# Performance work log

Measured on AMD Instinct MI355X. Metric: run time of the kernel, lower is better.

## Reference

```python
import jax, jax.numpy as jnp
import numpy as np

DIM = 192
HEADS = 6
HD = DIM // HEADS
WS = 7
R = 128  # low-rank projected sequence length
N_FULL = 3136  # 56*56
B = 32


def setup_inputs() -> dict:
    key = jax.random.key(0)
    ks = jax.random.split(key, 9)
    s = 0.02
    return {
        "x": jax.random.normal(ks[0], (2048, WS * WS, DIM), dtype=jnp.float32),
        "qkv_w": jax.random.normal(ks[1], (3 * DIM, DIM), dtype=jnp.float32) * s,
        "qkv_b": jax.random.normal(ks[2], (3 * DIM,), dtype=jnp.float32) * s,
        "E_w": jax.random.normal(ks[3], (R, N_FULL), dtype=jnp.float32) * s,
        "E_b": jax.random.normal(ks[4], (R,), dtype=jnp.float32) * s,
        "F_w": jax.random.normal(ks[5], (R, N_FULL), dtype=jnp.float32) * s,
        "F_b": jax.random.normal(ks[6], (R,), dtype=jnp.float32) * s,
        "proj_w": jax.random.normal(ks[7], (DIM, DIM), dtype=jnp.float32) * s,
        "proj_b": jax.random.normal(ks[8], (DIM,), dtype=jnp.float32) * s,
        "h": 56,
        "w": 56,
    }


def reference(x, qkv_w, qkv_b, E_w, E_b, F_w, F_b, proj_w, proj_b, h, w):
    C = x.shape[-1]
    # window_reverse: (nW*B, ws*ws, C) -> (B, H*W, C)
    xw = x.reshape(-1, WS, WS, C)
    b = xw.shape[0] // ((h // WS) * (w // WS))
    xm = xw.reshape(b, h // WS, w // WS, WS, WS, C)
    xm = xm.transpose(0, 1, 3, 2, 4, 5).reshape(b, h * w, C)
    n = h * w
    scale = 1.0 / np.sqrt(HD)

    qkv = (xm @ qkv_w.T + qkv_b).reshape(b, n, 3, HEADS, HD)
    qkv = qkv.transpose(2, 0, 3, 1, 4)  # (3, b, heads, n, hd)
    q, k, v = qkv[0] * scale, qkv[1], qkv[2]

    # Linformer low-rank projection along sequence: (b,h,n,d) -> (b,h,R,d)
    k_low = jnp.einsum('bhnd,kn->bhkd', k, E_w) + E_b[None, None, :, None]
    v_low = jnp.einsum('bhnd,kn->bhkd', v, F_w) + F_b[None, None, :, None]

    attn = jnp.einsum('bhnd,bhkd->bhnk', q, k_low)  # (b, heads, n, R)
    attn = jax.nn.softmax(attn, axis=-1)

    out = jnp.einsum('bhnk,bhkd->bhnd', attn, v_low)
    out = out.transpose(0, 2, 1, 3).reshape(b, n, C)
    out = out @ proj_w.T + proj_b
    return out
```

## Files before the change

kernel.cpp:

```cpp
#include <hip/hip_runtime.h>

typedef __bf16 bf16;
typedef bf16 bf16x8 __attribute__((ext_vector_type(8)));
typedef bf16 bf16x4 __attribute__((ext_vector_type(4)));
typedef float f32x4 __attribute__((ext_vector_type(4)));

#define MFMA16(a,b,c) __builtin_amdgcn_mfma_f32_16x16x32_bf16(a,b,c,0,0,0)

#define NSEQ 3136
#define CDIM 192

__device__ inline bf16x8 cvt8(float4 a, float4 b) {
  bf16x8 r;
  r[0]=(bf16)a.x; r[1]=(bf16)a.y; r[2]=(bf16)a.z; r[3]=(bf16)a.w;
  r[4]=(bf16)b.x; r[5]=(bf16)b.y; r[6]=(bf16)b.z; r[7]=(bf16)b.w;
  return r;
}

__device__ inline bf16x4 cvt4(float4 a) {
  bf16x4 r;
  r[0]=(bf16)a.x; r[1]=(bf16)a.y; r[2]=(bf16)a.z; r[3]=(bf16)a.w;
  return r;
}

__global__ void k_convert(const float* __restrict__ qkv_w, const float* __restrict__ E_w,
                          const float* __restrict__ F_w, const float* __restrict__ proj_w,
                          bf16* __restrict__ qkvw, bf16* __restrict__ EF, bf16* __restrict__ projw) {
  int i4 = blockIdx.x * blockDim.x + threadIdx.x;
  const int tot4 = 950272 / 4;
  for (; i4 < tot4; i4 += gridDim.x * blockDim.x) {
    int i = i4 * 4;
    float4 f;
    bf16* dst;
    if (i < 110592)      { f = *(const float4*)(qkv_w + i);            dst = qkvw + i; }
    else if (i < 512000) { f = *(const float4*)(E_w + (i - 110592));   dst = EF + (i - 110592); }
    else if (i < 913408) { f = *(const float4*)(F_w + (i - 512000));   dst = EF + (i - 110592); }
    else                 { f = *(const float4*)(proj_w + (i - 913408)); dst = projw + (i - 913408); }
    *(bf16x4*)dst = cvt4(f);
  }
}

__global__ void k_rowsum(const float* __restrict__ E_w, const float* __restrict__ F_w,
                         float* __restrict__ rowsums) {
  __shared__ float red[4];
  int row = blockIdx.x;
  const float* src = (row < 128) ? (E_w + (long)row * NSEQ) : (F_w + (long)(row - 128) * NSEQ);
  float s = 0.f;
  for (int i = threadIdx.x; i < 784; i += 256) {
    float4 f = *(const float4*)(src + i * 4);
    s += f.x + f.y + f.z + f.w;
  }
  for (int off = 32; off; off >>= 1) s += __shfl_xor(s, off);
  if ((threadIdx.x & 63) == 0) red[threadIdx.x >> 6] = s;
  __syncthreads();
  if (threadIdx.x == 0) rowsums[row] = red[0] + red[1] + red[2] + red[3];
}

__global__ void k_xT(const float* __restrict__ x, bf16* __restrict__ xmT) {
  __shared__ bf16 tile[64][196];
  int blk = blockIdx.x;
  int b = blk / 49, n0 = (blk % 49) * 64;
  int tid = threadIdx.x;
  for (int e = tid; e < 3072; e += 256) {
    int row = e / 48, c4 = e % 48;
    int n = n0 + row;
    int r = n / 56, cc = n % 56;
    long srcrow = (long)(b * 64 + (r / 7) * 8 + (cc / 7)) * 49 + (r % 7) * 7 + (cc % 7);
    float4 f = *(const float4*)(x + srcrow * 192 + c4 * 4);
    *(bf16x4*)&tile[row][c4 * 4] = cvt4(f);
  }
  __syncthreads();
  for (int e = tid; e < 1536; e += 256) {
    int c = e >> 3, k = e & 7;
    bf16x8 v;
    for (int jj = 0; jj < 8; jj++) v[jj] = tile[k * 8 + jj][c];
    *(bf16x8*)(xmT + ((long)b * 192 + c) * NSEQ + n0 + k * 8) = v;
  }
}

__launch_bounds__(512)
__global__ void k_xlow(const bf16* __restrict__ EF, const bf16* __restrict__ xmT,
                       float* __restrict__ partial) {
  __shared__ bf16 As[256][72];
  __shared__ bf16 Bs[192][72];
  int idx = blockIdx.x;
  int s = idx % 7, b = idx / 7;
  int kbase = s * 448;
  int tid = threadIdx.x;
  int wid = tid >> 6, lane = tid & 63;
  int wm = wid >> 2, wn = wid & 3;
  int lrow = lane & 15, hi = lane >> 4, lk = hi * 8;
  f32x4 zero = {0.f, 0.f, 0.f, 0.f};
  f32x4 acc[8][3];
  for (int i = 0; i < 8; i++) for (int j = 0; j < 3; j++) acc[i][j] = zero;
  for (int k0 = 0; k0 < 448; k0 += 64) {
    for (int i = 0; i < 4; i++) {
      int unit = i * 512 + tid;
      int row = unit >> 3, koff = (unit & 7) * 8;
      *(bf16x8*)&As[row][koff] = *(const bf16x8*)(EF + (long)row * NSEQ + kbase + k0 + koff);
    }
    for (int i = 0; i < 3; i++) {
      int unit = i * 512 + tid;
      int row = unit >> 3, koff = (unit & 7) * 8;
      *(bf16x8*)&Bs[row][koff] = *(const bf16x8*)(xmT + ((long)b * 192 + row) * NSEQ + kbase + k0 + koff);
    }
    __syncthreads();
    for (int ks = 0; ks < 2; ks++) {
      bf16x8 af[8], bfv[3];
      for (int i = 0; i < 8; i++) af[i]  = *(bf16x8*)&As[wm * 128 + 16 * i + lrow][ks * 32 + lk];
      for (int j = 0; j < 3; j++) bfv[j] = *(bf16x8*)&Bs[wn * 48 + 16 * j + lrow][ks * 32 + lk];
      for (int i = 0; i < 8; i++) for (int j = 0; j < 3; j++) acc[i][j] = MFMA16(af[i], bfv[j], acc[i][j]);
    }
    __syncthreads();
  }
  float* P = partial + (long)idx * 49152;
  for (int i = 0; i < 8; i++) for (int j = 0; j < 3; j++) for (int rr = 0; rr < 4; rr++) {
    int rl = wm * 128 + 16 * i + hi * 4 + rr;
    int cl = wn * 48 + 16 * j + lrow;
    P[rl * 192 + cl] = acc[i][j][rr];
  }
}

__global__ void k_reduce(const float* __restrict__ partial, bf16* __restrict__ el_fl) {
  int blk = blockIdx.x;
  int b = blk / 48, ch = blk % 48;
  long e = (long)ch * 1024 + threadIdx.x * 4;
  const float* P = partial + (long)b * 7 * 49152 + e;
  float4 sum = {0.f, 0.f, 0.f, 0.f};
  for (int s = 0; s < 7; s++) {
    float4 f = *(const float4*)(P + (long)s * 49152);
    sum.x += f.x; sum.y += f.y; sum.z += f.z; sum.w += f.w;
  }
  *(bf16x4*)(el_fl + (long)b * 49152 + e) = cvt4(sum);
}

__launch_bounds__(256)
__global__ void k_lowproj(const bf16* __restrict__ el_fl, const bf16* __restrict__ qkvw,
                          const float* __restrict__ qkv_b, const float* __restrict__ E_b,
                          const float* __restrict__ F_b, const float* __restrict__ rowsums,
                          bf16* __restrict__ k_low, bf16* __restrict__ v_lowT) {
  __shared__ bf16 As[64][200];
  __shared__ bf16 Bs[64][200];
  int idx = blockIdx.x;
  int b = idx / 12, rem = idx % 12;
  int type = rem / 6; rem %= 6;
  int bm, bn;
  if (type == 0) { bm = rem / 3; bn = rem % 3; }
  else           { bm = rem / 2; bn = rem % 2; }
  int m0 = bm * 64, n0 = bn * 64;
  int tid = threadIdx.x;
  int wid = tid >> 6, lane = tid & 63;
  int wm = wid >> 1, wn = wid & 1;
  int lrow = lane & 15, lk = (lane >> 4) * 8;
  int srow = tid >> 2, skoff = (tid & 3) * 16;
  const bf16* Ap; const bf16* Bp;
  if (type == 0) {
    Ap = el_fl + ((long)b * 256 + m0 + srow) * 192 + skoff;
    Bp = qkvw + (long)(192 + n0 + srow) * 192 + skoff;
  } else {
    Ap = qkvw + (long)(384 + m0 + srow) * 192 + skoff;
    Bp = el_fl + ((long)b * 256 + 128 + n0 + srow) * 192 + skoff;
  }
  for (int kk = 0; kk < 192; kk += 64) {
    *(bf16x8*)&As[srow][kk + skoff]     = *(const bf16x8*)(Ap + kk);
    *(bf16x8*)&As[srow][kk + skoff + 8] = *(const bf16x8*)(Ap + kk + 8);
    *(bf16x8*)&Bs[srow][kk + skoff]     = *(const bf16x8*)(Bp + kk);
    *(bf16x8*)&Bs[srow][kk + skoff + 8] = *(const bf16x8*)(Bp + kk + 8);
  }
  __syncthreads();
  f32x4 zero = {0.f, 0.f, 0.f, 0.f};
  f32x4 acc[2][2];
  for (int i = 0; i < 2; i++) for (int j = 0; j < 2; j++) acc[i][j] = zero;
  for (int ks = 0; ks < 6; ks++) {
    bf16x8 af[2], bfv[2];
    for (int i = 0; i < 2; i++) af[i]  = *(bf16x8*)&As[wm * 32 + 16 * i + lrow][ks * 32 + lk];
    for (int j = 0; j < 2; j++) bfv[j] = *(bf16x8*)&Bs[wn * 32 + 16 * j + lrow][ks * 32 + lk];
    for (int i = 0; i < 2; i++) for (int j = 0; j < 2; j++) acc[i][j] = MFMA16(af[i], bfv[j], acc[i][j]);
  }
  if (type == 0) {
    for (int i = 0; i < 2; i++) for (int j = 0; j < 2; j++) for (int rr = 0; rr < 4; rr++) {
      int kr = m0 + wm * 32 + 16 * i + (lane >> 4) * 4 + rr;
      int c = n0 + wn * 32 + 16 * j + lrow;
      float v = acc[i][j][rr] + rowsums[kr] * qkv_b[192 + c] + E_b[kr];
      k_low[((long)b * 128 + kr) * 192 + c] = (bf16)v;
    }
  } else {
    for (int i = 0; i < 2; i++) for (int j = 0; j < 2; j++) for (int rr = 0; rr < 4; rr++) {
      int c = m0 + wm * 32 + 16 * i + (lane >> 4) * 4 + rr;
      int kr = n0 + wn * 32 + 16 * j + lrow;
      float v = acc[i][j][rr] + rowsums[128 + kr] * qkv_b[384 + c] + F_b[kr];
      v_lowT[((long)b * 192 + c) * 128 + kr] = (bf16)v;
    }
  }
}

__launch_bounds__(256)
__global__ void k_qgemm2(const float* __restrict__ x, const bf16* __restrict__ qkvw,
                         const float* __restrict__ qkv_b, bf16* __restrict__ q) {
  __shared__ bf16 As[128][104];
  __shared__ bf16 Bs[192][200];
  long g0 = (long)blockIdx.x * 128;
  int tid = threadIdx.x;
  int wid = tid >> 6, lane = tid & 63;
  int lrow = lane & 15, lk = (lane >> 4) * 8;
  {
    int koff = (tid & 3) * 48;
    for (int r0 = 0; r0 < 192; r0 += 64) {
      int row = r0 + (tid >> 2);
      const bf16* Bp = qkvw + (long)row * 192 + koff;
      for (int m = 0; m < 6; m++)
        *(bf16x8*)&Bs[row][koff + 8 * m] = *(const bf16x8*)(Bp + 8 * m);
    }
  }
  int arow = tid >> 1, half = tid & 1;
  long g = g0 + arow;
  int b = (int)(g / NSEQ), n = (int)(g % NSEQ);
  int r = n / 56, cc = n % 56;
  long srcrow = (long)(b * 64 + (r / 7) * 8 + (cc / 7)) * 49 + (r % 7) * 7 + (cc % 7);
  const float* Ap = x + srcrow * 192 + half * 48;
  f32x4 zero = {0.f, 0.f, 0.f, 0.f};
  f32x4 acc[2][12];
  for (int i = 0; i < 2; i++) for (int j = 0; j < 12; j++) acc[i][j] = zero;
  for (int k0 = 0; k0 < 192; k0 += 96) {
    for (int m = 0; m < 3; m++) {
      const float4* xp = (const float4*)(Ap + k0 + 16 * m);
      float4 f0 = xp[0], f1 = xp[1];
      float4 f2 = xp[2], f3 = xp[3];
      *(bf16x8*)&As[arow][half * 48 + 16 * m] = cvt8(f0, f1);
      *(bf16x8*)&As[arow][half * 48 + 16 * m + 8] = cvt8(f2, f3);
    }
    __syncthreads();
    for (int ks = 0; ks < 3; ks++) {
      bf16x8 af[2];
      for (int i = 0; i < 2; i++) af[i] = *(bf16x8*)&As[wid * 32 + 16 * i + lrow][ks * 32 + lk];
      for (int j = 0; j < 12; j++) {
        bf16x8 bv = *(bf16x8*)&Bs[16 * j + lrow][k0 + ks * 32 + lk];
        acc[0][j] = MFMA16(af[0], bv, acc[0][j]);
        acc[1][j] = MFMA16(af[1], bv, acc[1][j]);
      }
    }
    __syncthreads();
  }
  const float scale = 0.17677669529663687f;
  for (int i = 0; i < 2; i++) for (int j = 0; j < 12; j++) for (int rr = 0; rr < 4; rr++) {
    long grow = g0 + wid * 32 + 16 * i + (lane >> 4) * 4 + rr;
    int c = 16 * j + lrow;
    float v = (acc[i][j][rr] + qkv_b[c]) * scale;
    q[grow * 192 + c] = (bf16)v;
  }
}

__launch_bounds__(256)
__global__ void k_attn(const bf16* __restrict__ q, const bf16* __restrict__ k_low,
                       const bf16* __restrict__ v_lowT, bf16* __restrict__ out_att) {
  __shared__ bf16 Ks[128][40];
  __shared__ bf16 Vs[32][136];
  __shared__ bf16 Ps[4][16][136];
  int idx = blockIdx.x;
  int nt = idx % 49, bh = idx / 49;
  int h = bh % 6, b = bh / 6;
  int n0 = nt * 64;
  int tid = threadIdx.x;
  int wid = tid >> 6, lane = tid & 63;
  int lrow = lane & 15, hi = lane >> 4, lk = hi * 8;
  {
    int row = tid >> 1, koff = (tid & 1) * 16;
    const bf16* src = k_low + ((long)b * 128 + row) * 192 + h * 32 + koff;
    *(bf16x8*)&Ks[row][koff] = *(const bf16x8*)src;
    *(bf16x8*)&Ks[row][koff + 8] = *(const bf16x8*)(src + 8);
  }
  {
    int row = tid >> 3, koff = (tid & 7) * 16;
    const bf16* src = v_lowT + ((long)b * 192 + h * 32 + row) * 128 + koff;
    *(bf16x8*)&Vs[row][koff] = *(const bf16x8*)src;
    *(bf16x8*)&Vs[row][koff + 8] = *(const bf16x8*)(src + 8);
  }
  int nrow = n0 + wid * 16 + lrow;
  bf16x8 qf = *(const bf16x8*)(q + ((long)b * NSEQ + nrow) * 192 + h * 32 + lk);
  __syncthreads();
  f32x4 zero = {0.f, 0.f, 0.f, 0.f};
  f32x4 s[8];
  for (int f = 0; f < 8; f++) {
    bf16x8 kf = *(bf16x8*)&Ks[16 * f + lrow][lk];
    s[f] = MFMA16(kf, qf, zero);
  }
  float m = s[0][0];
  for (int f = 0; f < 8; f++) for (int rr = 0; rr < 4; rr++) m = fmaxf(m, s[f][rr]);
  m = fmaxf(m, __shfl_xor(m, 16));
  m = fmaxf(m, __shfl_xor(m, 32));
  float sum = 0.f;
  for (int f = 0; f < 8; f++) for (int rr = 0; rr < 4; rr++) {
    float p = __expf(s[f][rr] - m);
    s[f][rr] = p; sum += p;
  }
  sum += __shfl_xor(sum, 16);
  sum += __shfl_xor(sum, 32);
  float inv = 1.0f / sum;
  for (int f = 0; f < 8; f++) {
    bf16x4 pv;
    for (int rr = 0; rr < 4; rr++) pv[rr] = (bf16)(s[f][rr] * inv);
    *(bf16x4*)&Ps[wid][lrow][16 * f + hi * 4] = pv;
  }
  __syncthreads();
  f32x4 o[2];
  o[0] = zero; o[1] = zero;
  for (int ks = 0; ks < 4; ks++) {
    bf16x8 pf = *(bf16x8*)&Ps[wid][lrow][ks * 32 + lk];
    for (int j = 0; j < 2; j++) {
      bf16x8 vf = *(bf16x8*)&Vs[16 * j + lrow][ks * 32 + lk];
      o[j] = MFMA16(pf, vf, o[j]);
    }
  }
  for (int j = 0; j < 2; j++) for (int rr = 0; rr < 4; rr++) {
    int nn = n0 + wid * 16 + hi * 4 + rr;
    out_att[((long)b * NSEQ + nn) * 192 + h * 32 + 16 * j + lrow] = (bf16)o[j][rr];
  }
}

__launch_bounds__(256)
__global__ void k_proj(const bf16* __restrict__ oa, const bf16* __restrict__ projw,
                       const float* __restrict__ proj_b, float* __restrict__ out) {
  __shared__ bf16 As[128][104];
  __shared__ bf16 Bs[192][200];
  long g0 = (long)blockIdx.x * 128;
  int tid = threadIdx.x;
  int wid = tid >> 6, lane = tid & 63;
  int lrow = lane & 15, lk = (lane >> 4) * 8;
  {
    int koff = (tid & 3) * 48;
    for (int r0 = 0; r0 < 192; r0 += 64) {
      int row = r0 + (tid >> 2);
      const bf16* Bp = projw + (long)row * 192 + koff;
      for (int m = 0; m < 6; m++)
        *(bf16x8*)&Bs[row][koff + 8 * m] = *(const bf16x8*)(Bp + 8 * m);
    }
  }
  int arow = tid >> 1, half = tid & 1;
  const bf16* Ap = oa + (g0 + arow) * 192 + half * 48;
  f32x4 zero = {0.f, 0.f, 0.f, 0.f};
  f32x4 acc[2][12];
  for (int i = 0; i < 2; i++) for (int j = 0; j < 12; j++) acc[i][j] = zero;
  for (int k0 = 0; k0 < 192; k0 += 96) {
    for (int m = 0; m < 6; m++)
      *(bf16x8*)&As[arow][half * 48 + 8 * m] = *(const bf16x8*)(Ap + k0 + 8 * m);
    __syncthreads();
    for (int ks = 0; ks < 3; ks++) {
      bf16x8 af[2];
      for (int i = 0; i < 2; i++) af[i] = *(bf16x8*)&As[wid * 32 + 16 * i + lrow][ks * 32 + lk];
      for (int j = 0; j < 12; j++) {
        bf16x8 bv = *(bf16x8*)&Bs[16 * j + lrow][k0 + ks * 32 + lk];
        acc[0][j] = MFMA16(af[0], bv, acc[0][j]);
        acc[1][j] = MFMA16(af[1], bv, acc[1][j]);
      }
    }
    __syncthreads();
  }
  for (int i = 0; i < 2; i++) for (int j = 0; j < 12; j++) for (int rr = 0; rr < 4; rr++) {
    long grow = g0 + wid * 32 + 16 * i + (lane >> 4) * 4 + rr;
    int c = 16 * j + lrow;
    out[grow * 192 + c] = acc[i][j][rr] + proj_b[c];
  }
}

extern "C" void kernel_launch(void* const* d_in, const int* in_sizes, int n_in,
                              void* d_out, int out_size, void* d_ws, size_t ws_size,
                              hipStream_t stream) {
  const float* x      = (const float*)d_in[0];
  const float* qkv_w  = (const float*)d_in[1];
  const float* qkv_b  = (const float*)d_in[2];
  const float* E_w    = (const float*)d_in[3];
  const float* E_b    = (const float*)d_in[4];
  const float* F_w    = (const float*)d_in[5];
  const float* F_b    = (const float*)d_in[6];
  const float* proj_w = (const float*)d_in[7];
  const float* proj_b = (const float*)d_in[8];
  float* out = (float*)d_out;

  char* ws = (char*)d_ws;
  size_t off = 0;
  auto alloc = [&](size_t bytes) { char* p = ws + off; off += (bytes + 255) & ~(size_t)255; return p; };
  bf16* qkvw     = (bf16*)alloc((size_t)110592 * 2);
  bf16* EF       = (bf16*)alloc((size_t)802816 * 2);
  bf16* projw    = (bf16*)alloc((size_t)36864 * 2);
  float* rowsums = (float*)alloc((size_t)256 * 4);
  bf16* xmT      = (bf16*)alloc((size_t)32 * 192 * NSEQ * 2);
  float* partial = (float*)alloc((size_t)224 * 49152 * 4);
  bf16* q        = (bf16*)partial;
  bf16* el_fl    = (bf16*)alloc((size_t)32 * 256 * 192 * 2);
  bf16* k_low    = (bf16*)alloc((size_t)32 * 128 * 192 * 2);
  bf16* v_lowT   = (bf16*)alloc((size_t)32 * 192 * 128 * 2);
  bf16* out_att  = xmT;

  k_convert<<<dim3(480), dim3(256), 0, stream>>>(qkv_w, E_w, F_w, proj_w, qkvw, EF, projw);
  k_rowsum<<<dim3(256), dim3(256), 0, stream>>>(E_w, F_w, rowsums);
  k_xT<<<dim3(32 * 49), dim3(256), 0, stream>>>(x, xmT);
  k_xlow<<<dim3(224), dim3(512), 0, stream>>>(EF, xmT, partial);
  k_reduce<<<dim3(1536), dim3(256), 0, stream>>>(partial, el_fl);
  k_lowproj<<<dim3(384), dim3(256), 0, stream>>>(el_fl, qkvw, qkv_b, E_b, F_b, rowsums, k_low, v_lowT);
  k_qgemm2<<<dim3(784), dim3(256), 0, stream>>>(x, qkvw, qkv_b, q);
  k_attn<<<dim3(32 * 6 * 49), dim3(256), 0, stream>>>(q, k_low, v_lowT, out_att);
  k_proj<<<dim3(784), dim3(256), 0, stream>>>(out_att, projw, proj_b, out);
}
```

Measured before the change: 300.5 us.

## Fuse Q projection into window-transpose kernel and merge weight prep kernels

Merges the weight conversion and rowsum kernels into one launch, and fuses the Q-projection GEMM into the window-reverse transpose kernel so x is read once from global memory and reused from shared memory. q now gets its own buffer instead of aliasing the partial buffer. k_low is stored head-major so attention loads contiguous per-head rows. This cuts launch count and a second full read of x, but the fused kernel uses more shared memory and a smaller 64-row tile, which may lower occupancy.

```diff
diff --git a/kernel.cpp b/kernel.cpp
--- a/kernel.cpp
+++ b/kernel.cpp
@@ -23,44 +23,51 @@
   return r;
 }
 
-__global__ void k_convert(const float* __restrict__ qkv_w, const float* __restrict__ E_w,
-                          const float* __restrict__ F_w, const float* __restrict__ proj_w,
-                          bf16* __restrict__ qkvw, bf16* __restrict__ EF, bf16* __restrict__ projw) {
-  int i4 = blockIdx.x * blockDim.x + threadIdx.x;
-  const int tot4 = 950272 / 4;
-  for (; i4 < tot4; i4 += gridDim.x * blockDim.x) {
-    int i = i4 * 4;
-    float4 f;
-    bf16* dst;
-    if (i < 110592)      { f = *(const float4*)(qkv_w + i);            dst = qkvw + i; }
-    else if (i < 512000) { f = *(const float4*)(E_w + (i - 110592));   dst = EF + (i - 110592); }
-    else if (i < 913408) { f = *(const float4*)(F_w + (i - 512000));   dst = EF + (i - 110592); }
-    else                 { f = *(const float4*)(proj_w + (i - 913408)); dst = projw + (i - 913408); }
-    *(bf16x4*)dst = cvt4(f);
-  }
-}
-
-__global__ void k_rowsum(const float* __restrict__ E_w, const float* __restrict__ F_w,
-                         float* __restrict__ rowsums) {
-  __shared__ float red[4];
-  int row = blockIdx.x;
-  const float* src = (row < 128) ? (E_w + (long)row * NSEQ) : (F_w + (long)(row - 128) * NSEQ);
-  float s = 0.f;
-  for (int i = threadIdx.x; i < 784; i += 256) {
-    float4 f = *(const float4*)(src + i * 4);
-    s += f.x + f.y + f.z + f.w;
-  }
-  for (int off = 32; off; off >>= 1) s += __shfl_xor(s, off);
-  if ((threadIdx.x & 63) == 0) red[threadIdx.x >> 6] = s;
-  __syncthreads();
-  if (threadIdx.x == 0) rowsums[row] = red[0] + red[1] + red[2] + red[3];
-}
-
-__global__ void k_xT(const float* __restrict__ x, bf16* __restrict__ xmT) {
+__global__ void k_prep(const float* __restrict__ qkv_w, const float* __restrict__ E_w,
+                       const float* __restrict__ F_w, const float* __restrict__ proj_w,
+                       bf16* __restrict__ qkvw, bf16* __restrict__ EF, bf16* __restrict__ projw,
+                       float* __restrict__ rowsums) {
+  if (blockIdx.x < 256) {
+    __shared__ float red[4];
+    int row = blockIdx.x;
+    const float* src = (row < 128) ? (E_w + (long)row * NSEQ) : (F_w + (long)(row - 128) * NSEQ);
+    float s = 0.f;
+    for (int i = threadIdx.x; i < 784; i += 256) {
+      float4 f = *(const float4*)(src + i * 4);
+      s += f.x + f.y + f.z + f.w;
+    }
+    for (int off = 32; off; off >>= 1) s += __shfl_xor(s, off);
+    if ((threadIdx.x & 63) == 0) red[threadIdx.x >> 6] = s;
+    __syncthreads();
+    if (threadIdx.x == 0) rowsums[row] = red[0] + red[1] + red[2] + red[3];
+  } else {
+    int i4 = (blockIdx.x - 256) * blockDim.x + threadIdx.x;
+    const int tot4 = 950272 / 4;
+    const int stride = 480 * 256;
+    for (; i4 < tot4; i4 += stride) {
+      int i = i4 * 4;
+      float4 f;
+      bf16* dst;
+      if (i < 110592)      { f = *(const float4*)(qkv_w + i);            dst = qkvw + i; }
+      else if (i < 512000) { f = *(const float4*)(E_w + (i - 110592));   dst = EF + (i - 110592); }
+      else if (i < 913408) { f = *(const float4*)(F_w + (i - 512000));   dst = EF + (i - 110592); }
+      else                 { f = *(const float4*)(proj_w + (i - 913408)); dst = projw + (i - 913408); }
+      *(bf16x4*)dst = cvt4(f);
+    }
+  }
+}
+
+__launch_bounds__(256)
+__global__ void k_xTq(const float* __restrict__ x, const bf16* __restrict__ qkvw,
+                      const float* __restrict__ qkv_b, bf16* __restrict__ xmT,
+                      bf16* __restrict__ q) {
   __shared__ bf16 tile[64][196];
+  __shared__ bf16 Bs[192][104];
   int blk = blockIdx.x;
   int b = blk / 49, n0 = (blk % 49) * 64;
   int tid = threadIdx.x;
+  int wid = tid >> 6, lane = tid & 63;
+  int lrow = lane & 15, hi = lane >> 4, lk = hi * 8;
   for (int e = tid; e < 3072; e += 256) {
     int row = e / 48, c4 = e % 48;
     int n = n0 + row;
@@ -69,12 +76,46 @@
     float4 f = *(const float4*)(x + srcrow * 192 + c4 * 4);
     *(bf16x4*)&tile[row][c4 * 4] = cvt4(f);
   }
-  __syncthreads();
+  for (int u = tid; u < 2304; u += 256) {
+    int row = u / 12, koff = (u % 12) * 8;
+    *(bf16x8*)&Bs[row][koff] = *(const bf16x8*)(qkvw + (long)row * 192 + koff);
+  }
+  __syncthreads();
+  f32x4 zero = {0.f, 0.f, 0.f, 0.f};
+  f32x4 acc[12];
+  for (int j = 0; j < 12; j++) acc[j] = zero;
+  for (int ks = 0; ks < 3; ks++) {
+    bf16x8 af = *(bf16x8*)&tile[wid * 16 + lrow][ks * 32 + lk];
+    for (int j = 0; j < 12; j++) {
+      bf16x8 bv = *(bf16x8*)&Bs[16 * j + lrow][ks * 32 + lk];
+      acc[j] = MFMA16(af, bv, acc[j]);
+    }
+  }
   for (int e = tid; e < 1536; e += 256) {
     int c = e >> 3, k = e & 7;
     bf16x8 v;
     for (int jj = 0; jj < 8; jj++) v[jj] = tile[k * 8 + jj][c];
     *(bf16x8*)(xmT + ((long)b * 192 + c) * NSEQ + n0 + k * 8) = v;
+  }
+  __syncthreads();
+  for (int u = tid; u < 2304; u += 256) {
+    int row = u / 12, koff = (u % 12) * 8;
+    *(bf16x8*)&Bs[row][koff] = *(const bf16x8*)(qkvw + (long)row * 192 + 96 + koff);
+  }
+  __syncthreads();
+  for (int ks = 0; ks < 3; ks++) {
+    bf16x8 af = *(bf16x8*)&tile[wid * 16 + lrow][96 + ks * 32 + lk];
+    for (int j = 0; j < 12; j++) {
+      bf16x8 bv = *(bf16x8*)&Bs[16 * j + lrow][ks * 32 + lk];
+      acc[j] = MFMA16(af, bv, acc[j]);
+    }
+  }
+  const float scale = 0.17677669529663687f;
+  for (int j = 0; j < 12; j++) for (int rr = 0; rr < 4; rr++) {
+    int rl = wid * 16 + hi * 4 + rr;
+    int c = 16 * j + lrow;
+    float v = (acc[j][rr] + qkv_b[c]) * scale;
+    q[((long)b * NSEQ + n0 + rl) * 192 + c] = (bf16)v;
   }
 }
 
@@ -138,7 +179,7 @@
 __global__ void k_lowproj(const bf16* __restrict__ el_fl, const bf16* __restrict__ qkvw,
                           const float* __restrict__ qkv_b, const float* __restrict__ E_b,
                           const float* __restrict__ F_b, const float* __restrict__ rowsums,
-                          bf16* __restrict__ k_low, bf16* __restrict__ v_lowT) {
+                          bf16* __restrict__ k_lowH, bf16* __restrict__ v_lowT) {
   __shared__ bf16 As[64][200];
   __shared__ bf16 Bs[64][200];
   int idx = blockIdx.x;
@@ -182,7 +223,7 @@
       int kr = m0 + wm * 32 + 16 * i + (lane >> 4) * 4 + rr;
       int c = n0 + wn * 32 + 16 * j + lrow;
       float v = acc[i][j][rr] + rowsums[kr] * qkv_b[192 + c] + E_b[kr];
-      k_low[((long)b * 128 + kr) * 192 + c] = (bf16)v;
+      k_lowH[(((long)b * 6 + (c >> 5)) * 128 + kr) * 32 + (c & 31)] = (bf16)v;
     }
   } else {
     for (int i = 0; i < 2; i++) for (int j = 0; j < 2; j++) for (int rr = 0; rr < 4; rr++) {
@@ -195,63 +236,7 @@
 }
 
 __launch_bounds__(256)
-__global__ void k_qgemm2(const float* __restrict__ x, const bf16* __restrict__ qkvw,
-                         const float* __restrict__ qkv_b, bf16* __restrict__ q) {
-  __shared__ bf16 As[128][104];
-  __shared__ bf16 Bs[192][200];
-  long g0 = (long)blockIdx.x * 128;
-  int tid = threadIdx.x;
-  int wid = tid >> 6, lane = tid & 63;
-  int lrow = lane & 15, lk = (lane >> 4) * 8;
-  {
-    int koff = (tid & 3) * 48;
-    for (int r0 = 0; r0 < 192; r0 += 64) {
-      int row = r0 + (tid >> 2);
-      const bf16* Bp = qkvw + (long)row * 192 + koff;
-      for (int m = 0; m < 6; m++)
-        *(bf16x8*)&Bs[row][koff + 8 * m] = *(const bf16x8*)(Bp + 8 * m);
-    }
-  }
-  int arow = tid >> 1, half = tid & 1;
-  long g = g0 + arow;
-  int b = (int)(g / NSEQ), n = (int)(g % NSEQ);
-  int r = n / 56, cc = n % 56;
-  long srcrow = (long)(b * 64 + (r / 7) * 8 + (cc / 7)) * 49 + (r % 7) * 7 + (cc % 7);
-  const float* Ap = x + srcrow * 192 + half * 48;
-  f32x4 zero = {0.f, 0.f, 0.f, 0.f};
-  f32x4 acc[2][12];
-  for (int i = 0; i < 2; i++) for (int j = 0; j < 12; j++) acc[i][j] = zero;
-  for (int k0 = 0; k0 < 192; k0 += 96) {
-    for (int m = 0; m < 3; m++) {
-      const float4* xp = (const float4*)(Ap + k0 + 16 * m);
-      float4 f0 = xp[0], f1 = xp[1];
-      float4 f2 = xp[2], f3 = xp[3];
-      *(bf16x8*)&As[arow][half * 48 + 16 * m] = cvt8(f0, f1);
-      *(bf16x8*)&As[arow][half * 48 + 16 * m + 8] = cvt8(f2, f3);
-    }
-    __syncthreads();
-    for (int ks = 0; ks < 3; ks++) {
-      bf16x8 af[2];
-      for (int i = 0; i < 2; i++) af[i] = *(bf16x8*)&As[wid * 32 + 16 * i + lrow][ks * 32 + lk];
-      for (int j = 0; j < 12; j++) {
-        bf16x8 bv = *(bf16x8*)&Bs[16 * j + lrow][k0 + ks * 32 + lk];
-        acc[0][j] = MFMA16(af[0], bv, acc[0][j]);
-        acc[1][j] = MFMA16(af[1], bv, acc[1][j]);
-      }
-    }
-    __syncthreads();
-  }
-  const float scale = 0.17677669529663687f;
-  for (int i = 0; i < 2; i++) for (int j = 0; j < 12; j++) for (int rr = 0; rr < 4; rr++) {
-    long grow = g0 + wid * 32 + 16 * i + (lane >> 4) * 4 + rr;
-    int c = 16 * j + lrow;
-    float v = (acc[i][j][rr] + qkv_b[c]) * scale;
-    q[grow * 192 + c] = (bf16)v;
-  }
-}
-
-__launch_bounds__(256)
-__global__ void k_attn(const bf16* __restrict__ q, const bf16* __restrict__ k_low,
+__global__ void k_attn(const bf16* __restrict__ q, const bf16* __restrict__ k_lowH,
                        const bf16* __restrict__ v_lowT, bf16* __restrict__ out_att) {
   __shared__ bf16 Ks[128][40];
   __shared__ bf16 Vs[32][136];
@@ -265,7 +250,7 @@
   int lrow = lane & 15, hi = lane >> 4, lk = hi * 8;
   {
     int row = tid >> 1, koff = (tid & 1) * 16;
-    const bf16* src = k_low + ((long)b * 128 + row) * 192 + h * 32 + koff;
+    const bf16* src = k_lowH + (((long)b * 6 + h) * 128 + row) * 32 + koff;
     *(bf16x8*)&Ks[row][koff] = *(const bf16x8*)src;
     *(bf16x8*)&Ks[row][koff + 8] = *(const bf16x8*)(src + 8);
   }
@@ -384,20 +369,18 @@
   bf16* projw    = (bf16*)alloc((size_t)36864 * 2);
   float* rowsums = (float*)alloc((size_t)256 * 4);
   bf16* xmT      = (bf16*)alloc((size_t)32 * 192 * NSEQ * 2);
+  bf16* q        = (bf16*)alloc((size_t)32 * NSEQ * 192 * 2);
   float* partial = (float*)alloc((size_t)224 * 49152 * 4);
-  bf16* q        = (bf16*)partial;
   bf16* el_fl    = (bf16*)alloc((size_t)32 * 256 * 192 * 2);
-  bf16* k_low    = (bf16*)alloc((size_t)32 * 128 * 192 * 2);
+  bf16* k_lowH   = (bf16*)alloc((size_t)32 * 6 * 128 * 32 * 2);
   bf16* v_lowT   = (bf16*)alloc((size_t)32 * 192 * 128 * 2);
   bf16* out_att  = xmT;
 
-  k_convert<<<dim3(480), dim3(256), 0, stream>>>(qkv_w, E_w, F_w, proj_w, qkvw, EF, projw);
-  k_rowsum<<<dim3(256), dim3(256), 0, stream>>>(E_w, F_w, rowsums);
-  k_xT<<<dim3(32 * 49), dim3(256), 0, stream>>>(x, xmT);
+  k_prep<<<dim3(736), dim3(256), 0, stream>>>(qkv_w, E_w, F_w, proj_w, qkvw, EF, projw, rowsums);
+  k_xTq<<<dim3(32 * 49), dim3(256), 0, stream>>>(x, qkvw, qkv_b, xmT, q);
   k_xlow<<<dim3(224), dim3(512), 0, stream>>>(EF, xmT, partial);
   k_reduce<<<dim3(1536), dim3(256), 0, stream>>>(partial, el_fl);
-  k_lowproj<<<dim3(384), dim3(256), 0, stream>>>(el_fl, qkvw, qkv_b, E_b, F_b, rowsums, k_low, v_lowT);
-  k_qgemm2<<<dim3(784), dim3(256), 0, stream>>>(x, qkvw, qkv_b, q);
-  k_attn<<<dim3(32 * 6 * 49), dim3(256), 0, stream>>>(q, k_low, v_lowT, out_att);
+  k_lowproj<<<dim3(384), dim3(256), 0, stream>>>(el_fl, qkvw, qkv_b, E_b, F_b, rowsums, k_lowH, v_lowT);
+  k_attn<<<dim3(32 * 6 * 49), dim3(256), 0, stream>>>(q, k_lowH, v_lowT, out_att);
   k_proj<<<dim3(784), dim3(256), 0, stream>>>(out_att, projw, proj_b, out);
 }
```

Result: faster. 293.2 us (-2.4%).
